# Performance work log

Hardware: AMD Instinct MI355X
Metric: run time of the kernel (lower is better)

Reference implementation:

```python
import jax, jax.numpy as jnp
import numpy as np

N_EMBDS = 1024
N_HEADS = 16
HEAD_DIM = N_EMBDS // N_HEADS


def setup_inputs() -> dict:
    key = jax.random.key(0)
    ks = jax.random.split(key, 5)
    B, T, C = 2, 2048, N_EMBDS
    x = jax.random.normal(ks[0], (B, T, C), dtype=jnp.float32)
    s = 1.0 / np.sqrt(C)
    W_attn = jax.random.normal(ks[1], (C, 3 * C), dtype=jnp.float32) * s
    b_attn = jnp.zeros((3 * C,), dtype=jnp.float32)
    W_proj = jax.random.normal(ks[2], (C, C), dtype=jnp.float32) * s
    b_proj = jnp.zeros((C,), dtype=jnp.float32)
    return {"x": x, "W_attn": W_attn, "b_attn": b_attn, "W_proj": W_proj, "b_proj": b_proj}


def reference(x, W_attn, b_attn, W_proj, b_proj):
    B, T, C = x.shape
    H, D = N_HEADS, HEAD_DIM
    qkv = x @ W_attn + b_attn  # [B, T, 3C]
    q, k, v = jnp.split(qkv, 3, axis=-1)
    # [B, H, T, D]
    q = q.reshape(B, T, H, D).transpose(0, 2, 1, 3)
    k = k.reshape(B, T, H, D).transpose(0, 2, 1, 3)
    v = v.reshape(B, T, H, D).transpose(0, 2, 1, 3)
    att = jnp.einsum('bhqd,bhkd->bhqk', q, k) * (1.0 / np.sqrt(D))  # [B,H,T,T]
    causal = jnp.tril(jnp.ones((T, T), dtype=bool))
    att = jnp.where(causal[None, None], att, -jnp.inf)
    att = jax.nn.softmax(att, axis=-1)
    y = jnp.einsum('bhqk,bhkd->bhqd', att, v)  # [B,H,T,D]
    y = y.transpose(0, 2, 1, 3).reshape(B, T, C)
    return y @ W_proj + b_proj
```

## Files before the change

### kernel.cpp

```cpp
#include <hip/hip_runtime.h>
#include <hip/hip_bf16.h>


typedef __bf16 bf16x8 __attribute__((ext_vector_type(8)));
typedef float  f32x4  __attribute__((ext_vector_type(4)));
#define BF16 __hip_bfloat16

constexpr int Bb = 2, Tt = 2048, Cc = 1024, Hh = 16, Dd = 64;
constexpr float NEG_INF = -1e30f;
constexpr float Q_SCALE = 0.18033688011112042f;
constexpr float EXP2_BIAS = 17.312340490667562f;

__device__ __forceinline__ f32x4 mfma16(bf16x8 a, bf16x8 b, f32x4 c) {
  return __builtin_amdgcn_mfma_f32_16x16x32_bf16(a, b, c, 0, 0, 0);
}

__device__ __forceinline__ float fast_exp2(float x) {
  float r;
  asm("v_exp_f32 %0, %1" : "=v"(r) : "v"(x));
  return r;
}

__device__ __forceinline__ void gll16(const void* g, void* l) {
  __builtin_amdgcn_global_load_lds((const __attribute__((address_space(1))) void*)g,
                                   (__attribute__((address_space(3))) void*)l,
                                   16, 0, 0);
}

__device__ __forceinline__ int kperm_inv7(int r) {
  return (r & 0x63) | ((r & 0x0C) << 1) | ((r & 0x10) >> 2);
}

__global__ void prep_kernel(const float* __restrict__ x, BF16* __restrict__ xb,
                            const float* __restrict__ Wa, BF16* __restrict__ WaT,
                            const float* __restrict__ Wp, BF16* __restrict__ WpT) {
  __shared__ float tile[32][33];
  const int bx = blockIdx.x, tid = threadIdx.x;
  if (bx < 2048) {
    const int i = (bx * 256 + tid) * 8;
    const float4 a = *(const float4*)&x[i];
    const float4 b = *(const float4*)&x[i + 4];
    BF16 o[8];
    o[0] = __float2bfloat16(a.x); o[1] = __float2bfloat16(a.y);
    o[2] = __float2bfloat16(a.z); o[3] = __float2bfloat16(a.w);
    o[4] = __float2bfloat16(b.x); o[5] = __float2bfloat16(b.y);
    o[6] = __float2bfloat16(b.z); o[7] = __float2bfloat16(b.w);
    *(uint4*)&xb[i] = *(const uint4*)o;
    return;
  }
  const float* in; BF16* outT; int K, N, gx, gy;
  if (bx < 5120) {
    const int idx = bx - 2048;
    in = Wa; outT = WaT; K = 1024; N = 3072; gx = idx % 96; gy = idx / 96;
  } else {
    const int idx = bx - 5120;
    in = Wp; outT = WpT; K = 1024; N = 1024; gx = idx % 32; gy = idx / 32;
  }
  const int n0 = gx * 32, k0 = gy * 32;
  const int tx = tid & 31, ty = tid >> 5;
#pragma unroll
  for (int i = ty; i < 32; i += 8) tile[i][tx] = in[(size_t)(k0 + i) * N + (n0 + tx)];
  __syncthreads();
#pragma unroll
  for (int i = ty; i < 32; i += 8)
    outT[(size_t)(n0 + i) * K + (k0 + tx)] = __float2bfloat16(tile[tx][i]);
}

template <int MODE>
__global__ __launch_bounds__(256) void gemm_bt(const BF16* __restrict__ A,
                                               const BF16* __restrict__ Bt,
                                               const float* __restrict__ bias,
                                               BF16* __restrict__ oq,
                                               BF16* __restrict__ ok,
                                               BF16* __restrict__ ov,
                                               float* __restrict__ fout,
                                               int Ndim, int Kdim) {
  __shared__ alignas(16) BF16 sA[128 * 64];
  __shared__ alignas(16) BF16 sB[128 * 64];
  const int tid = threadIdx.x;
  const int wave = tid >> 6, lane = tid & 63;
  const int quad = lane >> 4, l16 = lane & 15;
  const int wm = (wave >> 1) * 64, wn = (wave & 1) * 64;
  const int bm = blockIdx.y * 128, bn = blockIdx.x * 128;
  const int sw = l16 & 7;

  f32x4 acc[4][4];
#pragma unroll
  for (int i = 0; i < 4; ++i)
#pragma unroll
    for (int j = 0; j < 4; ++j) acc[i][j] = f32x4{0.f, 0.f, 0.f, 0.f};

  const int srow = wave * 32 + (lane >> 3);
  const int sgl = (lane ^ (lane >> 3)) & 7;
  const BF16* gA0 = &A[(size_t)(bm + srow) * Kdim + sgl * 8];
  const BF16* gB0 = &Bt[(size_t)(bn + srow) * Kdim + sgl * 8];
  const size_t rstep8 = (size_t)8 * Kdim;

  for (int k0 = 0; k0 < Kdim; k0 += 64) {
    __syncthreads();
#pragma unroll
    for (int s = 0; s < 4; ++s) {
      gll16(gA0 + s * rstep8 + k0, &sA[wave * 2048 + s * 512]);
      gll16(gB0 + s * rstep8 + k0, &sB[wave * 2048 + s * 512]);
    }
    __syncthreads();

#pragma unroll
    for (int h = 0; h < 2; ++h) {
      bf16x8 af[4], bf_[4];
#pragma unroll
      for (int i = 0; i < 4; ++i)
        af[i] = *(const bf16x8*)
            &sA[(wm + i * 16 + l16) * 64 + (((h * 4 + quad) ^ sw) << 3)];
#pragma unroll
      for (int j = 0; j < 4; ++j)
        bf_[j] = *(const bf16x8*)
            &sB[(wn + j * 16 + l16) * 64 + (((h * 4 + quad) ^ sw) << 3)];
#pragma unroll
      for (int i = 0; i < 4; ++i)
#pragma unroll
        for (int j = 0; j < 4; ++j) acc[i][j] = mfma16(af[i], bf_[j], acc[i][j]);
    }
  }

#pragma unroll
  for (int j = 0; j < 4; ++j) {
    const int gn = bn + wn + j * 16 + l16;
    const float bsv = bias[gn];
    if (MODE == 1) {
#pragma unroll
      for (int i = 0; i < 4; ++i)
#pragma unroll
        for (int r = 0; r < 4; ++r) {
          const int gm = bm + wm + i * 16 + quad * 4 + r;
          fout[(size_t)gm * Ndim + gn] = acc[i][j][r] + bsv;
        }
    } else {
      const int which = (bn + wn + j * 16) >> 10;
      const int c = gn & 1023;
      const int hh = c >> 6, dd = c & 63;
#pragma unroll
      for (int i = 0; i < 4; ++i) {
        const int gm0 = bm + wm + i * 16 + quad * 4;
        const int bb = gm0 >> 11, tk0 = gm0 & 2047;
        const size_t bh = (size_t)(bb * Hh + hh);
        if (which == 2) {
          BF16 tmp[4];
#pragma unroll
          for (int r = 0; r < 4; ++r) tmp[r] = __float2bfloat16(acc[i][j][r] + bsv);
          *(uint2*)&ov[(bh * Dd + dd) * Tt + tk0] = *(const uint2*)tmp;
        } else {
          BF16* dst = (which == 0) ? oq : ok;
          const float scale = (which == 0) ? Q_SCALE : 1.0f;
#pragma unroll
          for (int r = 0; r < 4; ++r)
            dst[(bh * Tt + tk0 + r) * Dd + dd] =
                __float2bfloat16((acc[i][j][r] + bsv) * scale);
        }
      }
    }
  }
}

__global__ __launch_bounds__(256) void attn_kernel(const BF16* __restrict__ qg,
                                                   const BF16* __restrict__ kg,
                                                   const BF16* __restrict__ vtg,
                                                   BF16* __restrict__ yb) {
  __shared__ alignas(16) BF16 sK[2 * 8192];
  __shared__ alignas(16) BF16 sV[2 * 8192];
  const int id = blockIdx.x;
  const int xcd = id & 7, local = id >> 3;
  const int bh = xcd * 4 + (local & 3);
  const int s = 31 - (local >> 2);
  const int b = bh >> 4, h = bh & 15;
  const int tid = threadIdx.x;
  const int wave = tid >> 6, lane = tid & 63;
  const int quad = lane >> 4, l16 = lane & 15;
  const size_t base = ((size_t)(b * Hh + h)) * Tt * Dd;
  const int qrow0 = s * 64 + wave * 16;
  const int sw = l16 & 7;

  bf16x8 qf0, qf1;
  {
    const size_t off = base + (size_t)(qrow0 + l16) * Dd;
    qf0 = *(const bf16x8*)&qg[off + quad * 8];
    qf1 = *(const bf16x8*)&qg[off + 32 + quad * 8];
  }

  bf16x8 ones8;
#pragma unroll
  for (int j = 0; j < 8; ++j) ones8[j] = (__bf16)1.0f;

  f32x4 o[4], oL;
#pragma unroll
  for (int i = 0; i < 4; ++i) o[i] = f32x4{0.f, 0.f, 0.f, 0.f};
  oL = f32x4{0.f, 0.f, 0.f, 0.f};

  const f32x4 cbias = f32x4{-EXP2_BIAS, -EXP2_BIAS, -EXP2_BIAS, -EXP2_BIAS};

  const int t = tid;
  const int sgk = (t ^ (t >> 3)) & 7;
  const int sgv = (t ^ (t >> 4)) & 15;
  const BF16* pk[4];
  const BF16* pv[4];
#pragma unroll
  for (int i = 0; i < 4; ++i) {
    pk[i] = &kg[base + (size_t)kperm_inv7(i * 32 + (t >> 3)) * Dd + sgk * 8];
    pv[i] = &vtg[base + (size_t)(i * 16 + (t >> 4)) * Tt + sgv * 8];
  }

#define STAGE(buf, jt_)                                            \
  do {                                                             \
    const size_t ko_ = (size_t)(jt_) * (128 * Dd);                 \
    const int vo_ = (jt_) * 128;                                   \
    _Pragma("unroll") for (int i_ = 0; i_ < 4; ++i_) {             \
      gll16(pk[i_] + ko_, &sK[(buf) * 8192 + i_ * 2048 + t * 8]);  \
      gll16(pv[i_] + vo_, &sV[(buf) * 8192 + i_ * 2048 + t * 8]);  \
    }                                                              \
  } while (0)

  const int nt = (s + 2) >> 1;
  STAGE(0, 0);

  for (int jt = 0; jt < nt; ++jt) {
    asm volatile("s_waitcnt vmcnt(0)" ::: "memory");
    __builtin_amdgcn_s_barrier();
    const BF16* sKb = &sK[(jt & 1) * 8192];
    const BF16* sVb = &sV[(jt & 1) * 8192];
    if (jt < nt - 1) STAGE((jt + 1) & 1, jt + 1);

    f32x4 sS[8];
    __builtin_amdgcn_s_setprio(1);
#pragma unroll
    for (int tt = 0; tt < 8; ++tt) {
      const bf16x8 kf0 =
          *(const bf16x8*)&sKb[(tt * 16 + l16) * 64 + ((quad ^ sw) << 3)];
      const bf16x8 kf1 =
          *(const bf16x8*)&sKb[(tt * 16 + l16) * 64 + (((4 + quad) ^ sw) << 3)];
      sS[tt] = mfma16(kf0, qf0, cbias);
      sS[tt] = mfma16(kf1, qf1, sS[tt]);
    }
    __builtin_amdgcn_s_setprio(0);

    if (jt == nt - 1) {
      const int q = qrow0 + l16;
      const int kb = jt * 128;
#pragma unroll
      for (int tt = 0; tt < 8; ++tt) {
        const int kc0 = kb + (tt >> 1) * 32 + quad * 8 + (tt & 1) * 4;
#pragma unroll
        for (int r = 0; r < 4; ++r)
          if (kc0 + r > q) sS[tt][r] = NEG_INF;
      }
    }

    bf16x8 pf[4];
#pragma unroll
    for (int cc = 0; cc < 4; ++cc)
#pragma unroll
      for (int j = 0; j < 8; ++j)
        pf[cc][j] = (__bf16)fast_exp2(sS[cc * 2 + (j >> 2)][j & 3]);

    __builtin_amdgcn_s_setprio(1);
#pragma unroll
    for (int cc = 0; cc < 4; ++cc) {
#pragma unroll
      for (int dt = 0; dt < 4; ++dt) {
        const bf16x8 vb = *(const bf16x8*)
            &sVb[(dt * 16 + l16) * 128 + ((((cc * 4 + quad) ^ l16) & 15) << 3)];
        o[dt] = mfma16(pf[cc], vb, o[dt]);
      }
      oL = mfma16(pf[cc], ones8, oL);
    }
    __builtin_amdgcn_s_setprio(0);
  }
#undef STAGE

#pragma unroll
  for (int r = 0; r < 4; ++r) {
    const float inv = 1.0f / oL[r];
    const int trow = qrow0 + quad * 4 + r;
#pragma unroll
    for (int dt = 0; dt < 4; ++dt)
      yb[((size_t)(b * Tt + trow)) * Cc + h * Dd + dt * 16 + l16] =
          __float2bfloat16(o[dt][r] * inv);
  }
}

extern "C" void kernel_launch(void* const* d_in, const int* in_sizes, int n_in,
                              void* d_out, int out_size, void* d_ws, size_t ws_size,
                              hipStream_t stream) {
  (void)in_sizes; (void)n_in; (void)out_size; (void)ws_size;
  const float* x      = (const float*)d_in[0];
  const float* W_attn = (const float*)d_in[1];
  const float* b_attn = (const float*)d_in[2];
  const float* W_proj = (const float*)d_in[3];
  const float* b_proj = (const float*)d_in[4];
  float* out = (float*)d_out;

  constexpr size_t SZ_WA = (size_t)3072 * 1024;
  constexpr size_t SZ_WP = (size_t)1024 * 1024;
  constexpr size_t SZ_X  = (size_t)4096 * 1024;
  constexpr size_t SZ_T  = (size_t)Bb * Hh * Tt * Dd;

  BF16* ws   = (BF16*)d_ws;
  BF16* wtAb = ws;
  BF16* wtPb = wtAb + SZ_WA;
  BF16* xb   = wtPb + SZ_WP;
  BF16* q    = xb + SZ_X;
  BF16* k    = q + SZ_T;
  BF16* vt   = k + SZ_T;
  BF16* yb   = vt + SZ_T;

  prep_kernel<<<dim3(6144), 256, 0, stream>>>(x, xb, W_attn, wtAb, W_proj, wtPb);
  gemm_bt<0><<<dim3(24, 32), 256, 0, stream>>>(xb, wtAb, b_attn, q, k, vt, nullptr,
                                               3072, 1024);
  attn_kernel<<<dim3(1024), 256, 0, stream>>>(q, k, vt, yb);
  gemm_bt<1><<<dim3(8, 32), 256, 0, stream>>>(yb, wtPb, b_proj, nullptr, nullptr,
                                              nullptr, out, 1024, 1024);
}
```

Baseline: 173.1 us.

## Process 128 query rows per attention block to reuse K/V tiles

Each attention block now handles 128 query rows instead of 64, with every wave computing two 16-row query groups against the same K/V shared-memory tiles. This halves the grid and the global K/V loads per query row, and amortises LDS fragment reads across twice the MFMA work. The cost is more registers per wave (two sets of scores, probabilities and accumulators), fewer blocks for load balancing, and coarser causal-mask granularity that wastes some work on the diagonal tile.

```diff
diff --git a/kernel.cpp b/kernel.cpp
--- a/kernel.cpp
+++ b/kernel.cpp
@@ -171,30 +171,35 @@
   const int id = blockIdx.x;
   const int xcd = id & 7, local = id >> 3;
   const int bh = xcd * 4 + (local & 3);
-  const int s = 31 - (local >> 2);
+  const int s = 15 - (local >> 2);
   const int b = bh >> 4, h = bh & 15;
   const int tid = threadIdx.x;
   const int wave = tid >> 6, lane = tid & 63;
   const int quad = lane >> 4, l16 = lane & 15;
   const size_t base = ((size_t)(b * Hh + h)) * Tt * Dd;
-  const int qrow0 = s * 64 + wave * 16;
+  const int qrow0 = s * 128 + wave * 32;
   const int sw = l16 & 7;
 
-  bf16x8 qf0, qf1;
-  {
-    const size_t off = base + (size_t)(qrow0 + l16) * Dd;
-    qf0 = *(const bf16x8*)&qg[off + quad * 8];
-    qf1 = *(const bf16x8*)&qg[off + 32 + quad * 8];
+  bf16x8 qf[2][2];
+#pragma unroll
+  for (int qg2 = 0; qg2 < 2; ++qg2) {
+    const size_t off = base + (size_t)(qrow0 + qg2 * 16 + l16) * Dd;
+    qf[qg2][0] = *(const bf16x8*)&qg[off + quad * 8];
+    qf[qg2][1] = *(const bf16x8*)&qg[off + 32 + quad * 8];
   }
 
   bf16x8 ones8;
 #pragma unroll
   for (int j = 0; j < 8; ++j) ones8[j] = (__bf16)1.0f;
 
-  f32x4 o[4], oL;
-#pragma unroll
-  for (int i = 0; i < 4; ++i) o[i] = f32x4{0.f, 0.f, 0.f, 0.f};
-  oL = f32x4{0.f, 0.f, 0.f, 0.f};
+  f32x4 o0[4], o1[4], oL0, oL1;
+#pragma unroll
+  for (int i = 0; i < 4; ++i) {
+    o0[i] = f32x4{0.f, 0.f, 0.f, 0.f};
+    o1[i] = f32x4{0.f, 0.f, 0.f, 0.f};
+  }
+  oL0 = f32x4{0.f, 0.f, 0.f, 0.f};
+  oL1 = f32x4{0.f, 0.f, 0.f, 0.f};
 
   const f32x4 cbias = f32x4{-EXP2_BIAS, -EXP2_BIAS, -EXP2_BIAS, -EXP2_BIAS};
 
@@ -219,7 +224,7 @@
     }                                                              \
   } while (0)
 
-  const int nt = (s + 2) >> 1;
+  const int nt = s + 1;
   STAGE(0, 0);
 
   for (int jt = 0; jt < nt; ++jt) {
@@ -229,7 +234,7 @@
     const BF16* sVb = &sV[(jt & 1) * 8192];
     if (jt < nt - 1) STAGE((jt + 1) & 1, jt + 1);
 
-    f32x4 sS[8];
+    f32x4 sS0[8], sS1[8];
     __builtin_amdgcn_s_setprio(1);
 #pragma unroll
     for (int tt = 0; tt < 8; ++tt) {
@@ -237,29 +242,35 @@
           *(const bf16x8*)&sKb[(tt * 16 + l16) * 64 + ((quad ^ sw) << 3)];
       const bf16x8 kf1 =
           *(const bf16x8*)&sKb[(tt * 16 + l16) * 64 + (((4 + quad) ^ sw) << 3)];
-      sS[tt] = mfma16(kf0, qf0, cbias);
-      sS[tt] = mfma16(kf1, qf1, sS[tt]);
+      sS0[tt] = mfma16(kf0, qf[0][0], cbias);
+      sS0[tt] = mfma16(kf1, qf[0][1], sS0[tt]);
+      sS1[tt] = mfma16(kf0, qf[1][0], cbias);
+      sS1[tt] = mfma16(kf1, qf[1][1], sS1[tt]);
     }
     __builtin_amdgcn_s_setprio(0);
 
     if (jt == nt - 1) {
-      const int q = qrow0 + l16;
       const int kb = jt * 128;
+      const int q0 = qrow0 + l16, q1 = qrow0 + 16 + l16;
 #pragma unroll
       for (int tt = 0; tt < 8; ++tt) {
         const int kc0 = kb + (tt >> 1) * 32 + quad * 8 + (tt & 1) * 4;
 #pragma unroll
-        for (int r = 0; r < 4; ++r)
-          if (kc0 + r > q) sS[tt][r] = NEG_INF;
+        for (int r = 0; r < 4; ++r) {
+          if (kc0 + r > q0) sS0[tt][r] = NEG_INF;
+          if (kc0 + r > q1) sS1[tt][r] = NEG_INF;
+        }
       }
     }
 
-    bf16x8 pf[4];
+    bf16x8 pf0[4], pf1[4];
 #pragma unroll
     for (int cc = 0; cc < 4; ++cc)
 #pragma unroll
-      for (int j = 0; j < 8; ++j)
-        pf[cc][j] = (__bf16)fast_exp2(sS[cc * 2 + (j >> 2)][j & 3]);
+      for (int j = 0; j < 8; ++j) {
+        pf0[cc][j] = (__bf16)fast_exp2(sS0[cc * 2 + (j >> 2)][j & 3]);
+        pf1[cc][j] = (__bf16)fast_exp2(sS1[cc * 2 + (j >> 2)][j & 3]);
+      }
 
     __builtin_amdgcn_s_setprio(1);
 #pragma unroll
@@ -268,9 +279,11 @@
       for (int dt = 0; dt < 4; ++dt) {
         const bf16x8 vb = *(const bf16x8*)
             &sVb[(dt * 16 + l16) * 128 + ((((cc * 4 + quad) ^ l16) & 15) << 3)];
-        o[dt] = mfma16(pf[cc], vb, o[dt]);
+        o0[dt] = mfma16(pf0[cc], vb, o0[dt]);
+        o1[dt] = mfma16(pf1[cc], vb, o1[dt]);
       }
-      oL = mfma16(pf[cc], ones8, oL);
+      oL0 = mfma16(pf0[cc], ones8, oL0);
+      oL1 = mfma16(pf1[cc], ones8, oL1);
     }
     __builtin_amdgcn_s_setprio(0);
   }
@@ -278,12 +291,17 @@
 
 #pragma unroll
   for (int r = 0; r < 4; ++r) {
-    const float inv = 1.0f / oL[r];
-    const int trow = qrow0 + quad * 4 + r;
-#pragma unroll
-    for (int dt = 0; dt < 4; ++dt)
-      yb[((size_t)(b * Tt + trow)) * Cc + h * Dd + dt * 16 + l16] =
-          __float2bfloat16(o[dt][r] * inv);
+    const float inv0 = 1.0f / oL0[r];
+    const float inv1 = 1.0f / oL1[r];
+    const int trow0 = qrow0 + quad * 4 + r;
+    const int trow1 = trow0 + 16;
+#pragma unroll
+    for (int dt = 0; dt < 4; ++dt) {
+      yb[((size_t)(b * Tt + trow0)) * Cc + h * Dd + dt * 16 + l16] =
+          __float2bfloat16(o0[dt][r] * inv0);
+      yb[((size_t)(b * Tt + trow1)) * Cc + h * Dd + dt * 16 + l16] =
+          __float2bfloat16(o1[dt][r] * inv1);
+    }
   }
 }
 
@@ -315,7 +333,7 @@
   prep_kernel<<<dim3(6144), 256, 0, stream>>>(x, xb, W_attn, wtAb, W_proj, wtPb);
   gemm_bt<0><<<dim3(24, 32), 256, 0, stream>>>(xb, wtAb, b_attn, q, k, vt, nullptr,
                                                3072, 1024);
-  attn_kernel<<<dim3(1024), 256, 0, stream>>>(q, k, vt, yb);
+  attn_kernel<<<dim3(512), 256, 0, stream>>>(q, k, vt, yb);
   gemm_bt<1><<<dim3(8, 32), 256, 0, stream>>>(yb, wtPb, b_proj, nullptr, nullptr,
                                               nullptr, out, 1024, 1024);
 }
```

Measured after the change: 175.0 us. Within noise of the previous version (+1.1%).

## Software-pipeline attention loop: overlap QK of next tile with PV of previous

Applied to the files above, without the earlier changes.

The attention inner loop is restructured so that each iteration computes QK^T for tile jt while running the PV accumulation for tile jt-1. K and V staging are split so V is fetched one iteration behind K, with double buffers guarded by barriers. The aim is to interleave the two MFMA phases with the exp and LDS work and to hide load latency. In exchange it adds a prologue and epilogue, keeps extra live registers (sS and pf across phases), and may raise register pressure.

```diff
diff --git a/kernel.cpp b/kernel.cpp
--- a/kernel.cpp
+++ b/kernel.cpp
@@ -209,72 +209,103 @@
     pv[i] = &vtg[base + (size_t)(i * 16 + (t >> 4)) * Tt + sgv * 8];
   }
 
-#define STAGE(buf, jt_)                                            \
-  do {                                                             \
-    const size_t ko_ = (size_t)(jt_) * (128 * Dd);                 \
-    const int vo_ = (jt_) * 128;                                   \
-    _Pragma("unroll") for (int i_ = 0; i_ < 4; ++i_) {             \
-      gll16(pk[i_] + ko_, &sK[(buf) * 8192 + i_ * 2048 + t * 8]);  \
-      gll16(pv[i_] + vo_, &sV[(buf) * 8192 + i_ * 2048 + t * 8]);  \
-    }                                                              \
+#define STAGE_K(buf, tt_)                                            \
+  do {                                                               \
+    const size_t ko_ = (size_t)(tt_) * 8192;                         \
+    _Pragma("unroll") for (int i_ = 0; i_ < 4; ++i_)                 \
+        gll16(pk[i_] + ko_, &sK[(buf) * 8192 + i_ * 2048 + t * 8]);  \
+  } while (0)
+#define STAGE_V(buf, tt_)                                            \
+  do {                                                               \
+    const int vo_ = (tt_) * 128;                                     \
+    _Pragma("unroll") for (int i_ = 0; i_ < 4; ++i_)                 \
+        gll16(pv[i_] + vo_, &sV[(buf) * 8192 + i_ * 2048 + t * 8]);  \
+  } while (0)
+
+#define QK_TILE(jt_)                                                        \
+  do {                                                                      \
+    const BF16* sKb_ = &sK[((jt_) & 1) * 8192];                             \
+    __builtin_amdgcn_s_setprio(1);                                          \
+    _Pragma("unroll") for (int tt = 0; tt < 8; ++tt) {                      \
+      const bf16x8 kf0 =                                                    \
+          *(const bf16x8*)&sKb_[(tt * 16 + l16) * 64 + ((quad ^ sw) << 3)]; \
+      const bf16x8 kf1 = *(const bf16x8*)                                   \
+          &sKb_[(tt * 16 + l16) * 64 + (((4 + quad) ^ sw) << 3)];           \
+      sS[tt] = mfma16(kf0, qf0, cbias);                                     \
+      sS[tt] = mfma16(kf1, qf1, sS[tt]);                                    \
+    }                                                                       \
+    __builtin_amdgcn_s_setprio(0);                                          \
+  } while (0)
+
+#define MASK_TILE(jt_)                                                  \
+  do {                                                                  \
+    const int kb_ = (jt_) * 128;                                        \
+    const int q_ = qrow0 + l16;                                         \
+    _Pragma("unroll") for (int tt = 0; tt < 8; ++tt) {                  \
+      const int kc0 = kb_ + (tt >> 1) * 32 + quad * 8 + (tt & 1) * 4;   \
+      _Pragma("unroll") for (int r = 0; r < 4; ++r)                     \
+          if (kc0 + r > q_) sS[tt][r] = NEG_INF;                        \
+    }                                                                   \
+  } while (0)
+
+#define EXP_P()                                                         \
+  do {                                                                  \
+    _Pragma("unroll") for (int cc = 0; cc < 4; ++cc)                    \
+        _Pragma("unroll") for (int j = 0; j < 8; ++j)                   \
+            pf[cc][j] = (__bf16)fast_exp2(sS[cc * 2 + (j >> 2)][j & 3]); \
+  } while (0)
+
+#define PV_TILE(jt_)                                                          \
+  do {                                                                        \
+    const BF16* sVb_ = &sV[((jt_) & 1) * 8192];                               \
+    __builtin_amdgcn_s_setprio(1);                                            \
+    _Pragma("unroll") for (int cc = 0; cc < 4; ++cc) {                        \
+      _Pragma("unroll") for (int dt = 0; dt < 4; ++dt) {                      \
+        const bf16x8 vb = *(const bf16x8*)                                    \
+            &sVb_[(dt * 16 + l16) * 128 +                                     \
+                  ((((cc * 4 + quad) ^ l16) & 15) << 3)];                     \
+        o[dt] = mfma16(pf[cc], vb, o[dt]);                                    \
+      }                                                                       \
+      oL = mfma16(pf[cc], ones8, oL);                                         \
+    }                                                                         \
+    __builtin_amdgcn_s_setprio(0);                                            \
   } while (0)
 
   const int nt = (s + 2) >> 1;
-  STAGE(0, 0);
-
-  for (int jt = 0; jt < nt; ++jt) {
+  f32x4 sS[8];
+  bf16x8 pf[4];
+
+  STAGE_K(0, 0);
+
+  asm volatile("s_waitcnt vmcnt(0)" ::: "memory");
+  __builtin_amdgcn_s_barrier();
+  STAGE_V(0, 0);
+  if (nt > 1) STAGE_K(1, 1);
+  QK_TILE(0);
+  if (nt == 1) MASK_TILE(0);
+
+  for (int jt = 1; jt < nt; ++jt) {
     asm volatile("s_waitcnt vmcnt(0)" ::: "memory");
     __builtin_amdgcn_s_barrier();
-    const BF16* sKb = &sK[(jt & 1) * 8192];
-    const BF16* sVb = &sV[(jt & 1) * 8192];
-    if (jt < nt - 1) STAGE((jt + 1) & 1, jt + 1);
-
-    f32x4 sS[8];
-    __builtin_amdgcn_s_setprio(1);
-#pragma unroll
-    for (int tt = 0; tt < 8; ++tt) {
-      const bf16x8 kf0 =
-          *(const bf16x8*)&sKb[(tt * 16 + l16) * 64 + ((quad ^ sw) << 3)];
-      const bf16x8 kf1 =
-          *(const bf16x8*)&sKb[(tt * 16 + l16) * 64 + (((4 + quad) ^ sw) << 3)];
-      sS[tt] = mfma16(kf0, qf0, cbias);
-      sS[tt] = mfma16(kf1, qf1, sS[tt]);
-    }
-    __builtin_amdgcn_s_setprio(0);
-
-    if (jt == nt - 1) {
-      const int q = qrow0 + l16;
-      const int kb = jt * 128;
-#pragma unroll
-      for (int tt = 0; tt < 8; ++tt) {
-        const int kc0 = kb + (tt >> 1) * 32 + quad * 8 + (tt & 1) * 4;
-#pragma unroll
-        for (int r = 0; r < 4; ++r)
-          if (kc0 + r > q) sS[tt][r] = NEG_INF;
-      }
-    }
-
-    bf16x8 pf[4];
-#pragma unroll
-    for (int cc = 0; cc < 4; ++cc)
-#pragma unroll
-      for (int j = 0; j < 8; ++j)
-        pf[cc][j] = (__bf16)fast_exp2(sS[cc * 2 + (j >> 2)][j & 3]);
-
-    __builtin_amdgcn_s_setprio(1);
-#pragma unroll
-    for (int cc = 0; cc < 4; ++cc) {
-#pragma unroll
-      for (int dt = 0; dt < 4; ++dt) {
-        const bf16x8 vb = *(const bf16x8*)
-            &sVb[(dt * 16 + l16) * 128 + ((((cc * 4 + quad) ^ l16) & 15) << 3)];
-        o[dt] = mfma16(pf[cc], vb, o[dt]);
-      }
-      oL = mfma16(pf[cc], ones8, oL);
-    }
-    __builtin_amdgcn_s_setprio(0);
-  }
-#undef STAGE
+    STAGE_V(jt & 1, jt);
+    if (jt + 1 < nt) STAGE_K((jt + 1) & 1, jt + 1);
+    EXP_P();
+    QK_TILE(jt);
+    if (jt == nt - 1) MASK_TILE(jt);
+    PV_TILE(jt - 1);
+  }
+
+  asm volatile("s_waitcnt vmcnt(0)" ::: "memory");
+  __builtin_amdgcn_s_barrier();
+  EXP_P();
+  PV_TILE(nt - 1);
+
+#undef STAGE_K
+#undef STAGE_V
+#undef QK_TILE
+#undef MASK_TILE
+#undef EXP_P
+#undef PV_TILE
 
 #pragma unroll
   for (int r = 0; r < 4; ++r) {
```

Measured after the change: 167.4 us. 1.03x faster.
